# Kernel tuning notes

Hardware: AMD Instinct MI355X
Metric: run time of the kernel (lower is better)

## Reference

```python
import jax, jax.numpy as jnp
import numpy as np
import math

D_MODEL = 1024
N_HEADS = 16
D_HEAD = 64
VOCAB = 32000
MAX_SEQ = 2048
PAD_TOKEN = 0
EPS = 1e-5
NEG = -1000000000.0


def layer_norm(x, g, b):
    m = jnp.mean(x, axis=-1, keepdims=True)
    v = jnp.mean(jnp.square(x - m), axis=-1, keepdims=True)
    return (x - m) * jax.lax.rsqrt(v + EPS) * g + b


def setup_inputs() -> dict:
    key = jax.random.key(0)
    ks = jax.random.split(key, 12)
    s = 0.02
    inp = {
        "tokens": jax.random.randint(ks[0], (2, 2048), 0, VOCAB, dtype=jnp.int64)
            if jax.config.jax_enable_x64 else jax.random.randint(ks[0], (2, 2048), 0, VOCAB, dtype=jnp.int32),
        "emb": jax.random.normal(ks[1], (VOCAB, D_MODEL), jnp.float32) * s,
        "pos_emb": jax.random.normal(ks[2], (MAX_SEQ, D_MODEL), jnp.float32) * s,
        "ln1_g": jnp.ones((D_MODEL,), jnp.float32), "ln1_b": jnp.zeros((D_MODEL,), jnp.float32),
        "ln2_g": jnp.ones((D_MODEL,), jnp.float32), "ln2_b": jnp.zeros((D_MODEL,), jnp.float32),
        "ln3_g": jnp.ones((D_MODEL,), jnp.float32), "ln3_b": jnp.zeros((D_MODEL,), jnp.float32),
        "Wq": jax.random.normal(ks[3], (D_MODEL, N_HEADS * D_HEAD), jnp.float32) * s,
        "bq": jnp.zeros((N_HEADS * D_HEAD,), jnp.float32),
        "Wk": jax.random.normal(ks[4], (D_MODEL, N_HEADS * D_HEAD), jnp.float32) * s,
        "bk": jnp.zeros((N_HEADS * D_HEAD,), jnp.float32),
        "Wv": jax.random.normal(ks[5], (D_MODEL, N_HEADS * D_HEAD), jnp.float32) * s,
        "bv": jnp.zeros((N_HEADS * D_HEAD,), jnp.float32),
        "Wo": jax.random.normal(ks[6], (N_HEADS * D_HEAD, D_MODEL), jnp.float32) * s,
        "bo": jnp.zeros((D_MODEL,), jnp.float32),
        "W1": jax.random.normal(ks[7], (D_MODEL, 4 * D_MODEL), jnp.float32) * s,
        "b1": jnp.zeros((4 * D_MODEL,), jnp.float32),
        "W2": jax.random.normal(ks[8], (4 * D_MODEL, D_MODEL), jnp.float32) * s,
        "b2": jnp.zeros((D_MODEL,), jnp.float32),
    }
    return inp


def reference(tokens, emb, pos_emb, ln1_g, ln1_b, ln2_g, ln2_b, ln3_g, ln3_b,
              Wq, bq, Wk, bk, Wv, bv, Wo, bo, W1, b1, W2, b2):
    b, s = tokens.shape
    # embedding + learned positional embedding
    x = emb[tokens] + pos_emb[jnp.arange(s)][None, :, :]  # [b,s,d]
    x = layer_norm(x, ln1_g, ln1_b)
    Q = (x @ Wq + bq).reshape(b, s, N_HEADS, D_HEAD).transpose(0, 2, 1, 3)  # [b,n,s,d]
    K = (x @ Wk + bk).reshape(b, s, N_HEADS, D_HEAD).transpose(0, 2, 1, 3)
    V = (x @ Wv + bv).reshape(b, s, N_HEADS, D_HEAD).transpose(0, 2, 1, 3)
    logits = jnp.einsum('bnsd,bntd->bnst', Q, K) / math.sqrt(D_HEAD)  # [b,n,s,s]
    causal = jnp.triu(jnp.full((s, s), NEG, jnp.float32), k=1)
    pad_mask = jnp.where(tokens == PAD_TOKEN, NEG, 0.0)  # keys masked: [b,s]
    logits = logits + causal[None, None, :, :] + pad_mask[:, None, None, :]
    probs = jax.nn.softmax(logits, axis=-1)
    attn = jnp.einsum('bnst,bntd->bnsd', probs, V)
    attn = attn.transpose(0, 2, 1, 3).reshape(b, s, N_HEADS * D_HEAD)
    attn_out = attn @ Wo + bo
    x = x + layer_norm(attn_out, ln2_g, ln2_b)
    h = jax.nn.gelu(layer_norm(x, ln3_g, ln3_b) @ W1 + b1, approximate=False)
    x = x + (h @ W2 + b2)
    return x
```

## Files before the change

### kernel.cpp

```cpp
#include <hip/hip_runtime.h>
#include <cstdint>
#include <cstddef>


#define SEQ     2048
#define NTOK    4096
#define DMODEL  1024
#define NHEAD   16
#define DHEAD   64
#define MASKV   (-30.0f)
#define LN_EPS  1e-5f

typedef __bf16 bf16_t;
typedef __bf16 bf16x8 __attribute__((ext_vector_type(8)));
typedef float  f32x4  __attribute__((ext_vector_type(4)));

#define MFMA_BF16(a,b,c) __builtin_amdgcn_mfma_f32_16x16x32_bf16((a),(b),(c),0,0,0)

__device__ __forceinline__ void gload_lds16(const void* g, void* l) {
  __builtin_amdgcn_global_load_lds(
      (__attribute__((address_space(1))) void*)(g),
      (__attribute__((address_space(3))) void*)(l), 16, 0, 0);
}

__global__ __launch_bounds__(256)
void wtrans_kernel(const float* __restrict__ W, bf16_t* __restrict__ WT,
                   int K, int N) {
  __shared__ float tile[64][65];
  const int n0 = blockIdx.x * 64, k0 = blockIdx.y * 64;
  const int c = threadIdx.x & 63, rb = threadIdx.x >> 6;
#pragma unroll
  for (int i = 0; i < 16; ++i) {
    int r = i * 4 + rb;
    tile[r][c] = W[(size_t)(k0 + r) * N + n0 + c];
  }
  __syncthreads();
#pragma unroll
  for (int i = 0; i < 16; ++i) {
    int r = i * 4 + rb;
    WT[(size_t)(n0 + r) * K + k0 + c] = (bf16_t)tile[c][r];
  }
}

__global__ __launch_bounds__(256)
void pack_bias_kernel(const float* __restrict__ bq, const float* __restrict__ bk,
                      const float* __restrict__ bv, float* __restrict__ o) {
  int i = blockIdx.x * 256 + threadIdx.x;
  if (i < 1024) { o[i] = bq[i]; o[1024 + i] = bk[i]; o[2048 + i] = bv[i]; }
}

__global__ __launch_bounds__(256)
void ln1_kernel(const int* __restrict__ tokens, const float* __restrict__ emb,
                const float* __restrict__ pos, const float* __restrict__ g,
                const float* __restrict__ bb, float* __restrict__ xln,
                bf16_t* __restrict__ xlnb) {
  __shared__ float red[8];
  const int t = blockIdx.x;
  const int s = t & (SEQ - 1);
  const int tok = tokens[t];
  const int d0 = threadIdx.x * 4;
  const int w = threadIdx.x >> 6, lane = threadIdx.x & 63;

  float4 e  = *(const float4*)(emb + (size_t)tok * DMODEL + d0);
  float4 pp = *(const float4*)(pos + (size_t)s   * DMODEL + d0);
  float x0 = e.x + pp.x, x1 = e.y + pp.y, x2v = e.z + pp.z, x3v = e.w + pp.w;
  float s1 = x0 + x1 + x2v + x3v;
  float s2 = x0*x0 + x1*x1 + x2v*x2v + x3v*x3v;
#pragma unroll
  for (int o = 32; o >= 1; o >>= 1) { s1 += __shfl_xor(s1, o); s2 += __shfl_xor(s2, o); }
  if (lane == 0) { red[w] = s1; red[4 + w] = s2; }
  __syncthreads();
  s1 = red[0] + red[1] + red[2] + red[3];
  s2 = red[4] + red[5] + red[6] + red[7];
  float mean = s1 * (1.0f / DMODEL);
  float var  = s2 * (1.0f / DMODEL) - mean * mean;
  float inv  = rsqrtf(var + LN_EPS);
  float4 gv = *(const float4*)(g + d0);
  float4 bv = *(const float4*)(bb + d0);
  float y0 = (x0  - mean) * inv * gv.x + bv.x;
  float y1 = (x1  - mean) * inv * gv.y + bv.y;
  float y2 = (x2v - mean) * inv * gv.z + bv.z;
  float y3 = (x3v - mean) * inv * gv.w + bv.w;
  *(float4*)(xln + (size_t)t * DMODEL + d0) = make_float4(y0, y1, y2, y3);
  union { ushort4 u; bf16_t b[4]; } cv;
  cv.b[0] = (bf16_t)y0; cv.b[1] = (bf16_t)y1; cv.b[2] = (bf16_t)y2; cv.b[3] = (bf16_t)y3;
  *(ushort4*)(xlnb + (size_t)t * DMODEL + d0) = cv.u;
}

__global__ __launch_bounds__(256)
void ln23_kernel(const float* __restrict__ ao, const float* __restrict__ xln,
                 const float* __restrict__ g2, const float* __restrict__ bb2,
                 const float* __restrict__ g3, const float* __restrict__ bb3,
                 float* __restrict__ x2o, bf16_t* __restrict__ x3b) {
  __shared__ float red[8];
  const int t = blockIdx.x;
  const int d0 = threadIdx.x * 4;
  const int w = threadIdx.x >> 6, lane = threadIdx.x & 63;

  float4 a = *(const float4*)(ao + (size_t)t * DMODEL + d0);
  float s1 = a.x + a.y + a.z + a.w;
  float s2 = a.x*a.x + a.y*a.y + a.z*a.z + a.w*a.w;
#pragma unroll
  for (int o = 32; o >= 1; o >>= 1) { s1 += __shfl_xor(s1, o); s2 += __shfl_xor(s2, o); }
  if (lane == 0) { red[w] = s1; red[4 + w] = s2; }
  __syncthreads();
  s1 = red[0] + red[1] + red[2] + red[3];
  s2 = red[4] + red[5] + red[6] + red[7];
  float mean = s1 * (1.0f / DMODEL);
  float var  = s2 * (1.0f / DMODEL) - mean * mean;
  float inv  = rsqrtf(var + LN_EPS);
  float4 gv = *(const float4*)(g2 + d0);
  float4 bv = *(const float4*)(bb2 + d0);
  float4 xv = *(const float4*)(xln + (size_t)t * DMODEL + d0);
  float y0 = xv.x + (a.x - mean) * inv * gv.x + bv.x;
  float y1 = xv.y + (a.y - mean) * inv * gv.y + bv.y;
  float y2 = xv.z + (a.z - mean) * inv * gv.z + bv.z;
  float y3 = xv.w + (a.w - mean) * inv * gv.w + bv.w;
  *(float4*)(x2o + (size_t)t * DMODEL + d0) = make_float4(y0, y1, y2, y3);

  float t1 = y0 + y1 + y2 + y3;
  float t2 = y0*y0 + y1*y1 + y2*y2 + y3*y3;
#pragma unroll
  for (int o = 32; o >= 1; o >>= 1) { t1 += __shfl_xor(t1, o); t2 += __shfl_xor(t2, o); }
  __syncthreads();
  if (lane == 0) { red[w] = t1; red[4 + w] = t2; }
  __syncthreads();
  t1 = red[0] + red[1] + red[2] + red[3];
  t2 = red[4] + red[5] + red[6] + red[7];
  float mean2 = t1 * (1.0f / DMODEL);
  float var2  = t2 * (1.0f / DMODEL) - mean2 * mean2;
  float inv2  = rsqrtf(var2 + LN_EPS);
  float4 gv3 = *(const float4*)(g3 + d0);
  float4 bv3 = *(const float4*)(bb3 + d0);
  union { ushort4 u; bf16_t b[4]; } cv;
  cv.b[0] = (bf16_t)((y0 - mean2) * inv2 * gv3.x + bv3.x);
  cv.b[1] = (bf16_t)((y1 - mean2) * inv2 * gv3.y + bv3.y);
  cv.b[2] = (bf16_t)((y2 - mean2) * inv2 * gv3.z + bv3.z);
  cv.b[3] = (bf16_t)((y3 - mean2) * inv2 * gv3.w + bv3.w);
  *(ushort4*)(x3b + (size_t)t * DMODEL + d0) = cv.u;
}

constexpr int EPI_BF16 = 0, EPI_F32 = 1, EPI_GELU = 2, EPI_RES = 3;

template <int EPI>
__global__ __launch_bounds__(256, 2)
void gemm_bt(const bf16_t* __restrict__ A, const bf16_t* __restrict__ B,
             const float* __restrict__ bias, const float* __restrict__ res,
             bf16_t* __restrict__ obf, float* __restrict__ of32,
             int M, int N, int K) {
  __shared__ __attribute__((aligned(16))) bf16_t As[128 * 64];
  __shared__ __attribute__((aligned(16))) bf16_t Bs[128 * 64];
  const int tid = threadIdx.x;
  const int w = tid >> 6, lane = tid & 63;
  const int quad = lane >> 4, l16 = lane & 15;
  const int m0 = blockIdx.x * 128, n0 = blockIdx.y * 128;
  const int wm = (w >> 1) * 64, wn = (w & 1) * 64;
  const size_t Kz = (size_t)K;

  f32x4 acc[4][4] = {};

  const bf16_t* Ag = A + (size_t)(m0 + w * 32 + (lane >> 3)) * Kz + (lane & 7) * 8;
  const bf16_t* Bg = B + (size_t)(n0 + w * 32 + (lane >> 3)) * Kz + (lane & 7) * 8;
  bf16_t* Asw = &As[(w * 32) * 64];
  bf16_t* Bsw = &Bs[(w * 32) * 64];

  for (int k0 = 0; k0 < K; k0 += 64) {
#pragma unroll
    for (int i = 0; i < 4; ++i) {
      gload_lds16(Ag + (size_t)i * 8 * Kz + k0, Asw + i * 8 * 64);
      gload_lds16(Bg + (size_t)i * 8 * Kz + k0, Bsw + i * 8 * 64);
    }
    __syncthreads();
#pragma unroll
    for (int kc = 0; kc < 2; ++kc) {
      bf16x8 af[4], bfr[4];
#pragma unroll
      for (int i = 0; i < 4; ++i) {
        af[i]  = *(const bf16x8*)&As[(wm + i * 16 + l16) * 64 + kc * 32 + quad * 8];
        bfr[i] = *(const bf16x8*)&Bs[(wn + i * 16 + l16) * 64 + kc * 32 + quad * 8];
      }
#pragma unroll
      for (int mi = 0; mi < 4; ++mi)
#pragma unroll
        for (int ni = 0; ni < 4; ++ni)
          acc[mi][ni] = MFMA_BF16(af[mi], bfr[ni], acc[mi][ni]);
    }
    __syncthreads();
  }

#pragma unroll
  for (int ni = 0; ni < 4; ++ni) {
    const int col = n0 + wn + ni * 16 + l16;
    const float bv = bias[col];
#pragma unroll
    for (int mi = 0; mi < 4; ++mi) {
#pragma unroll
      for (int r = 0; r < 4; ++r) {
        const int row = m0 + wm + mi * 16 + quad * 4 + r;
        float v = acc[mi][ni][r] + bv;
        if constexpr (EPI == EPI_GELU)
          v = 0.5f * v * (1.0f + erff(v * 0.70710678118654752f));
        if constexpr (EPI == EPI_RES)
          v += res[(size_t)row * N + col];
        if constexpr (EPI == EPI_BF16 || EPI == EPI_GELU)
          obf[(size_t)row * N + col] = (bf16_t)v;
        else
          of32[(size_t)row * N + col] = v;
      }
    }
  }
}

__global__ __launch_bounds__(256)
void vtrans_kernel(const bf16_t* __restrict__ qkv, bf16_t* __restrict__ Vt) {
  __shared__ bf16_t tile[64][72];
  const int bh = blockIdx.y;
  const int b = bh >> 4, h = bh & 15;
  const int s0 = blockIdx.x * 64;
  const int c = threadIdx.x & 63, rb = threadIdx.x >> 6;
#pragma unroll
  for (int i = 0; i < 16; ++i) {
    int r = i * 4 + rb;
    tile[r][c] = qkv[(size_t)(b * SEQ + s0 + r) * 3072 + 2048 + h * 64 + c];
  }
  __syncthreads();
#pragma unroll
  for (int i = 0; i < 16; ++i) {
    int r = i * 4 + rb;
    Vt[((size_t)bh * 64 + r) * SEQ + s0 + c] = tile[c][r];
  }
}


__device__ __forceinline__ unsigned pack2_bf16(float e, float o) {
  union { bf16_t b; unsigned short s; } lo, hi;
  lo.b = (bf16_t)e; hi.b = (bf16_t)o;
  return (unsigned)lo.s | ((unsigned)hi.s << 16);
}

template <bool DIAG>
__device__ __forceinline__ void attn_tile(
    int k0, int chunkCnt, int w, int quad, int l16, int krow,
    const bf16_t* __restrict__ Kbase, const bf16_t* __restrict__ Vbase,
    const int* __restrict__ tokb,
    const bf16x8 (&qf)[2][2], bf16x8 onev,
    f32x4 (&oacc)[2][4], f32x4 (&lacc)[2]) {

  f32x4 sc0[8], sc1[8];

#pragma unroll
  for (int c = 0; c < 4; ++c)
    if (!DIAG || c < chunkCnt) {
      int4 t0 = *(const int4*)(tokb + k0 + 32 * c + 8 * quad);
      int4 t1 = *(const int4*)(tokb + k0 + 32 * c + 8 * quad + 4);
      f32x4 pe, po;
      pe[0] = (t0.x == 0) ? MASKV : 0.0f;
      po[0] = (t0.y == 0) ? MASKV : 0.0f;
      pe[1] = (t0.z == 0) ? MASKV : 0.0f;
      po[1] = (t0.w == 0) ? MASKV : 0.0f;
      pe[2] = (t1.x == 0) ? MASKV : 0.0f;
      po[2] = (t1.y == 0) ? MASKV : 0.0f;
      pe[3] = (t1.z == 0) ? MASKV : 0.0f;
      po[3] = (t1.w == 0) ? MASKV : 0.0f;
      sc0[2 * c] = pe; sc0[2 * c + 1] = po;
      sc1[2 * c] = pe; sc1[2 * c + 1] = po;
    }

#pragma unroll
  for (int kc = 0; kc < 2; ++kc)
#pragma unroll
    for (int ni = 0; ni < 8; ++ni)
      if (!DIAG || ni < 2 * chunkCnt) {
        bf16x8 kf = *(const bf16x8*)(Kbase
            + (size_t)(k0 + 32 * (ni >> 1) + (ni & 1) + krow) * 3072
            + kc * 32 + quad * 8);
        sc0[ni] = MFMA_BF16(kf, qf[0][kc], sc0[ni]);
        sc1[ni] = MFMA_BF16(kf, qf[1][kc], sc1[ni]);
      }

#pragma unroll
  for (int mi = 0; mi < 2; ++mi) {
    f32x4* sc = mi ? sc1 : sc0;
    const int ql = w * 32 + mi * 16 + l16;
#pragma unroll
    for (int ni = 0; ni < 8; ++ni)
      if (!DIAG || ni < 2 * chunkCnt) {
#pragma unroll
        for (int r = 0; r < 4; ++r) {
          float v = sc[ni][r];
          if (DIAG) {
            int keyl = 32 * (ni >> 1) + (ni & 1) + 8 * quad + 2 * r;
            if (keyl > ql) v += MASKV;
          }
          sc[ni][r] = __expf(v);
        }
      }
  }

#pragma unroll
  for (int c = 0; c < 4; ++c)
    if (!DIAG || c < chunkCnt) {
      union { unsigned u[4]; bf16x8 v; } pb0, pb1;
#pragma unroll
      for (int m = 0; m < 4; ++m) {
        pb0.u[m] = pack2_bf16(sc0[2 * c][m], sc0[2 * c + 1][m]);
        pb1.u[m] = pack2_bf16(sc1[2 * c][m], sc1[2 * c + 1][m]);
      }
      lacc[0] = MFMA_BF16(onev, pb0.v, lacc[0]);
      lacc[1] = MFMA_BF16(onev, pb1.v, lacc[1]);
#pragma unroll
      for (int nd = 0; nd < 4; ++nd) {
        bf16x8 vf = *(const bf16x8*)(Vbase
            + (size_t)(nd * 16 + l16) * SEQ + k0 + c * 32 + quad * 8);
        oacc[0][nd] = MFMA_BF16(vf, pb0.v, oacc[0][nd]);
        oacc[1][nd] = MFMA_BF16(vf, pb1.v, oacc[1][nd]);
      }
    }
}

__global__ __launch_bounds__(256, 2)
void attn_kernel(const bf16_t* __restrict__ qkv, const bf16_t* __restrict__ Vt,
                 const int* __restrict__ tokens, bf16_t* __restrict__ attnb) {
  const int tid = threadIdx.x;
  const int w = tid >> 6, lane = tid & 63;
  const int quad = lane >> 4, l16 = lane & 15;
  const int bh = blockIdx.x;
  const int by = (int)blockIdx.y;
  const int strip = (by < 8) ? (15 - by) : (by - 8);
  const int b = bh >> 4, h = bh & 15;
  const int ntiles = strip + 1;
  const int qrow0 = strip * 128 + w * 32;
  const int krow = ((l16 >> 2) << 3) + ((l16 & 3) << 1);

  const bf16_t* Kbase = qkv + (size_t)b * SEQ * 3072 + 1024 + h * 64;
  const bf16_t* Vbase = Vt + (size_t)bh * 64 * SEQ;
  const int*    tokb  = tokens + b * SEQ;

  bf16x8 qf[2][2];
#pragma unroll
  for (int mi = 0; mi < 2; ++mi) {
    const size_t trow = (size_t)(b * SEQ + qrow0 + mi * 16 + l16) * 3072 + h * 64;
    qf[mi][0] = *(const bf16x8*)(qkv + trow + quad * 8);
    qf[mi][1] = *(const bf16x8*)(qkv + trow + 32 + quad * 8);
  }
#pragma unroll
  for (int mi = 0; mi < 2; ++mi)
#pragma unroll
    for (int kc = 0; kc < 2; ++kc)
#pragma unroll
      for (int j = 0; j < 8; ++j)
        qf[mi][kc][j] = (bf16_t)((float)qf[mi][kc][j] * 0.125f);

  bf16x8 onev;
#pragma unroll
  for (int j = 0; j < 8; ++j) onev[j] = (bf16_t)1.0f;

  f32x4 oacc[2][4] = {};
  f32x4 lacc[2] = {};

  for (int kt = 0; kt < ntiles - 1; ++kt)
    attn_tile<false>(kt * 128, 4, w, quad, l16, krow,
                     Kbase, Vbase, tokb, qf, onev, oacc, lacc);
  attn_tile<true>((ntiles - 1) * 128, w + 1, w, quad, l16, krow,
                  Kbase, Vbase, tokb, qf, onev, oacc, lacc);

#pragma unroll
  for (int mi = 0; mi < 2; ++mi) {
    const float invl = 1.0f / lacc[mi][0];
    const size_t row =
        (size_t)(b * SEQ + qrow0 + mi * 16 + l16) * DMODEL + h * 64;
#pragma unroll
    for (int nd = 0; nd < 4; ++nd) {
      union { ushort4 u; bf16_t bv[4]; } cv;
#pragma unroll
      for (int r = 0; r < 4; ++r)
        cv.bv[r] = (bf16_t)(oacc[mi][nd][r] * invl);
      *(ushort4*)(attnb + row + nd * 16 + quad * 4) = cv.u;
    }
  }
}

extern "C" void kernel_launch(void* const* d_in, const int* in_sizes, int n_in,
                              void* d_out, int out_size, void* d_ws, size_t ws_size,
                              hipStream_t stream) {
  const int*   tokens = (const int*)d_in[0];
  const float* emb    = (const float*)d_in[1];
  const float* pos    = (const float*)d_in[2];
  const float* ln1g   = (const float*)d_in[3];
  const float* ln1b   = (const float*)d_in[4];
  const float* ln2g   = (const float*)d_in[5];
  const float* ln2b   = (const float*)d_in[6];
  const float* ln3g   = (const float*)d_in[7];
  const float* ln3b   = (const float*)d_in[8];
  const float* Wq     = (const float*)d_in[9];
  const float* bq     = (const float*)d_in[10];
  const float* Wk     = (const float*)d_in[11];
  const float* bk     = (const float*)d_in[12];
  const float* Wv     = (const float*)d_in[13];
  const float* bv     = (const float*)d_in[14];
  const float* Wo     = (const float*)d_in[15];
  const float* bo     = (const float*)d_in[16];
  const float* W1     = (const float*)d_in[17];
  const float* b1     = (const float*)d_in[18];
  const float* W2     = (const float*)d_in[19];
  const float* b2     = (const float*)d_in[20];
  float* out = (float*)d_out;

  char* p = (char*)d_ws;
  auto alloc = [&](size_t bytes) {
    char* q = p; p += (bytes + 255) & ~(size_t)255; return q;
  };
  float*  x_ln   = (float*)alloc((size_t)NTOK * DMODEL * 4);
  bf16_t* x_lnb  = (bf16_t*)alloc((size_t)NTOK * DMODEL * 2);
  bf16_t* WqkvT  = (bf16_t*)alloc((size_t)3072 * 1024 * 2);
  float*  bqkv   = (float*)alloc(3072 * 4);
  bf16_t* WoT    = (bf16_t*)alloc((size_t)1024 * 1024 * 2);
  bf16_t* W1T    = (bf16_t*)alloc((size_t)4096 * 1024 * 2);
  bf16_t* W2T    = (bf16_t*)alloc((size_t)1024 * 4096 * 2);
  bf16_t* qkvb   = (bf16_t*)alloc((size_t)NTOK * 3072 * 2);
  bf16_t* Vtb    = (bf16_t*)alloc((size_t)32 * 64 * SEQ * 2);
  bf16_t* attnb  = (bf16_t*)alloc((size_t)NTOK * DMODEL * 2);
  float*  attn_o = (float*)alloc((size_t)NTOK * DMODEL * 4);
  float*  x2     = (float*)alloc((size_t)NTOK * DMODEL * 4);
  bf16_t* x3b    = (bf16_t*)alloc((size_t)NTOK * DMODEL * 2);
  bf16_t* hbuf   = (bf16_t*)alloc((size_t)NTOK * 4096 * 2);

  wtrans_kernel<<<dim3(16, 16), 256, 0, stream>>>(Wq, WqkvT,                 1024, 1024);
  wtrans_kernel<<<dim3(16, 16), 256, 0, stream>>>(Wk, WqkvT + 1024ull * 1024, 1024, 1024);
  wtrans_kernel<<<dim3(16, 16), 256, 0, stream>>>(Wv, WqkvT + 2048ull * 1024, 1024, 1024);
  wtrans_kernel<<<dim3(16, 16), 256, 0, stream>>>(Wo, WoT, 1024, 1024);
  wtrans_kernel<<<dim3(64, 16), 256, 0, stream>>>(W1, W1T, 1024, 4096);
  wtrans_kernel<<<dim3(16, 64), 256, 0, stream>>>(W2, W2T, 4096, 1024);
  pack_bias_kernel<<<4, 256, 0, stream>>>(bq, bk, bv, bqkv);

  ln1_kernel<<<NTOK, 256, 0, stream>>>(tokens, emb, pos, ln1g, ln1b, x_ln, x_lnb);

  gemm_bt<EPI_BF16><<<dim3(32, 24), 256, 0, stream>>>(
      x_lnb, WqkvT, bqkv, nullptr, qkvb, nullptr, NTOK, 3072, 1024);

  vtrans_kernel<<<dim3(32, 32), 256, 0, stream>>>(qkvb, Vtb);

  attn_kernel<<<dim3(32, 16), 256, 0, stream>>>(qkvb, Vtb, tokens, attnb);

  gemm_bt<EPI_F32><<<dim3(32, 8), 256, 0, stream>>>(
      attnb, WoT, bo, nullptr, nullptr, attn_o, NTOK, 1024, 1024);

  ln23_kernel<<<NTOK, 256, 0, stream>>>(attn_o, x_ln, ln2g, ln2b, ln3g, ln3b, x2, x3b);

  gemm_bt<EPI_GELU><<<dim3(32, 32), 256, 0, stream>>>(
      x3b, W1T, b1, nullptr, hbuf, nullptr, NTOK, 4096, 1024);

  gemm_bt<EPI_RES><<<dim3(32, 8), 256, 0, stream>>>(
      hbuf, W2T, b2, x2, nullptr, out, NTOK, 1024, 4096);

  (void)in_sizes; (void)n_in; (void)out_size; (void)ws_size;
}
```

Before: 582.9 us.

## Stage K/V tiles in swizzled double-buffered LDS for attention

The attention kernel now copies each 128-key K tile and V^T tile into double-buffered LDS with asynchronous global-to-LDS loads. The next tile is prefetched while the current one is computed, and the per-wave redundant global reads are replaced by XOR-swizzled LDS reads. The V transpose kernel writes 128-key blocks in the matching swizzled layout with 16-byte stores. The pad mask is applied after QK instead of being used to seed the accumulators. In exchange, the kernel uses 64KB of LDS and adds a block barrier per tile, which may limit occupancy to 2 blocks per CU.

```diff
diff --git a/kernel.cpp b/kernel.cpp
--- a/kernel.cpp
+++ b/kernel.cpp
@@ -213,21 +213,26 @@
 
 __global__ __launch_bounds__(256)
 void vtrans_kernel(const bf16_t* __restrict__ qkv, bf16_t* __restrict__ Vt) {
-  __shared__ bf16_t tile[64][72];
+  __shared__ bf16_t tile[128][72];
   const int bh = blockIdx.y;
   const int b = bh >> 4, h = bh & 15;
-  const int s0 = blockIdx.x * 64;
+  const int s0 = blockIdx.x * 128;
   const int c = threadIdx.x & 63, rb = threadIdx.x >> 6;
 #pragma unroll
-  for (int i = 0; i < 16; ++i) {
+  for (int i = 0; i < 32; ++i) {
     int r = i * 4 + rb;
     tile[r][c] = qkv[(size_t)(b * SEQ + s0 + r) * 3072 + 2048 + h * 64 + c];
   }
   __syncthreads();
-#pragma unroll
-  for (int i = 0; i < 16; ++i) {
-    int r = i * 4 + rb;
-    Vt[((size_t)bh * 64 + r) * SEQ + s0 + c] = tile[c][r];
+  const int d = threadIdx.x >> 2;
+  const int k4 = threadIdx.x & 3;
+#pragma unroll
+  for (int kk = 0; kk < 4; ++kk) {
+    const int k = kk * 4 + k4;
+    union { uint4 u; bf16_t bv[8]; } vv;
+#pragma unroll
+    for (int e = 0; e < 8; ++e) vv.bv[e] = tile[k * 8 + e][d];
+    *(uint4*)(Vt + (size_t)(bh * 64 + d) * SEQ + s0 + ((k ^ (d & 7)) << 3)) = vv.u;
   }
 }
 
@@ -238,42 +243,39 @@
   return (unsigned)lo.s | ((unsigned)hi.s << 16);
 }
 
+__device__ __forceinline__ int tok_at(const int4& a, const int4& b, int j) {
+  switch (j) {
+    case 0: return a.x; case 1: return a.y; case 2: return a.z; case 3: return a.w;
+    case 4: return b.x; case 5: return b.y; case 6: return b.z; default: return b.w;
+  }
+}
+
 template <bool DIAG>
 __device__ __forceinline__ void attn_tile(
-    int k0, int chunkCnt, int w, int quad, int l16, int krow,
-    const bf16_t* __restrict__ Kbase, const bf16_t* __restrict__ Vbase,
+    const bf16_t* __restrict__ Ksb, const bf16_t* __restrict__ Vsb,
+    int k0, int chunkCnt, int w, int quad, int l16, int krow, int xr0,
     const int* __restrict__ tokb,
     const bf16x8 (&qf)[2][2], bf16x8 onev,
     f32x4 (&oacc)[2][4], f32x4 (&lacc)[2]) {
 
-  f32x4 sc0[8], sc1[8];
-
+  int4 tA[4], tB[4];
 #pragma unroll
   for (int c = 0; c < 4; ++c)
     if (!DIAG || c < chunkCnt) {
-      int4 t0 = *(const int4*)(tokb + k0 + 32 * c + 8 * quad);
-      int4 t1 = *(const int4*)(tokb + k0 + 32 * c + 8 * quad + 4);
-      f32x4 pe, po;
-      pe[0] = (t0.x == 0) ? MASKV : 0.0f;
-      po[0] = (t0.y == 0) ? MASKV : 0.0f;
-      pe[1] = (t0.z == 0) ? MASKV : 0.0f;
-      po[1] = (t0.w == 0) ? MASKV : 0.0f;
-      pe[2] = (t1.x == 0) ? MASKV : 0.0f;
-      po[2] = (t1.y == 0) ? MASKV : 0.0f;
-      pe[3] = (t1.z == 0) ? MASKV : 0.0f;
-      po[3] = (t1.w == 0) ? MASKV : 0.0f;
-      sc0[2 * c] = pe; sc0[2 * c + 1] = po;
-      sc1[2 * c] = pe; sc1[2 * c + 1] = po;
-    }
+      tA[c] = *(const int4*)(tokb + k0 + 32 * c + 8 * quad);
+      tB[c] = *(const int4*)(tokb + k0 + 32 * c + 8 * quad + 4);
+    }
+
+  f32x4 sc0[8] = {}, sc1[8] = {};
 
 #pragma unroll
   for (int kc = 0; kc < 2; ++kc)
 #pragma unroll
     for (int ni = 0; ni < 8; ++ni)
       if (!DIAG || ni < 2 * chunkCnt) {
-        bf16x8 kf = *(const bf16x8*)(Kbase
-            + (size_t)(k0 + 32 * (ni >> 1) + (ni & 1) + krow) * 3072
-            + kc * 32 + quad * 8);
+        const int r = 32 * (ni >> 1) + (ni & 1) + krow;
+        bf16x8 kf = *(const bf16x8*)&Ksb[r * 64
+            + (((kc * 4 + quad) ^ (xr0 + (ni & 1))) << 3)];
         sc0[ni] = MFMA_BF16(kf, qf[0][kc], sc0[ni]);
         sc1[ni] = MFMA_BF16(kf, qf[1][kc], sc1[ni]);
       }
@@ -285,11 +287,13 @@
 #pragma unroll
     for (int ni = 0; ni < 8; ++ni)
       if (!DIAG || ni < 2 * chunkCnt) {
+        const int c = ni >> 1, e = ni & 1;
 #pragma unroll
         for (int r = 0; r < 4; ++r) {
           float v = sc[ni][r];
+          if (tok_at(tA[c], tB[c], 2 * r + e) == 0) v += MASKV;
           if (DIAG) {
-            int keyl = 32 * (ni >> 1) + (ni & 1) + 8 * quad + 2 * r;
+            int keyl = 32 * c + e + 8 * quad + 2 * r;
             if (keyl > ql) v += MASKV;
           }
           sc[ni][r] = __expf(v);
@@ -310,8 +314,8 @@
       lacc[1] = MFMA_BF16(onev, pb1.v, lacc[1]);
 #pragma unroll
       for (int nd = 0; nd < 4; ++nd) {
-        bf16x8 vf = *(const bf16x8*)(Vbase
-            + (size_t)(nd * 16 + l16) * SEQ + k0 + c * 32 + quad * 8);
+        bf16x8 vf = *(const bf16x8*)&Vsb[(nd * 16 + l16) * 128
+            + (((c * 4 + quad) ^ (l16 & 7)) << 3)];
         oacc[0][nd] = MFMA_BF16(vf, pb0.v, oacc[0][nd]);
         oacc[1][nd] = MFMA_BF16(vf, pb1.v, oacc[1][nd]);
       }
@@ -321,6 +325,9 @@
 __global__ __launch_bounds__(256, 2)
 void attn_kernel(const bf16_t* __restrict__ qkv, const bf16_t* __restrict__ Vt,
                  const int* __restrict__ tokens, bf16_t* __restrict__ attnb) {
+  __shared__ __attribute__((aligned(16))) bf16_t Ks[2][128 * 64];
+  __shared__ __attribute__((aligned(16))) bf16_t Vs[2][64 * 128];
+
   const int tid = threadIdx.x;
   const int w = tid >> 6, lane = tid & 63;
   const int quad = lane >> 4, l16 = lane & 15;
@@ -331,6 +338,8 @@
   const int ntiles = strip + 1;
   const int qrow0 = strip * 128 + w * 32;
   const int krow = ((l16 >> 2) << 3) + ((l16 & 3) << 1);
+  const int xr0 = (l16 & 3) << 1;
+  const int sw_chunk = (lane & 7) ^ ((lane >> 3) & 7);
 
   const bf16_t* Kbase = qkv + (size_t)b * SEQ * 3072 + 1024 + h * 64;
   const bf16_t* Vbase = Vt + (size_t)bh * 64 * SEQ;
@@ -358,11 +367,35 @@
   f32x4 oacc[2][4] = {};
   f32x4 lacc[2] = {};
 
-  for (int kt = 0; kt < ntiles - 1; ++kt)
-    attn_tile<false>(kt * 128, 4, w, quad, l16, krow,
-                     Kbase, Vbase, tokb, qf, onev, oacc, lacc);
-  attn_tile<true>((ntiles - 1) * 128, w + 1, w, quad, l16, krow,
-                  Kbase, Vbase, tokb, qf, onev, oacc, lacc);
+  auto stage = [&](int bf, int k0) {
+    const bf16_t* Kg = Kbase + (size_t)(k0 + w * 32 + (lane >> 3)) * 3072
+                       + sw_chunk * 8;
+    bf16_t* Kl = &Ks[bf][(w * 32) * 64];
+#pragma unroll
+    for (int i = 0; i < 4; ++i)
+      gload_lds16(Kg + (size_t)i * 8 * 3072, Kl + i * 8 * 64);
+    const bf16_t* Vg = Vbase + (size_t)(w * 16 + (lane >> 4)) * SEQ + k0
+                       + (lane & 15) * 8;
+    bf16_t* Vl = &Vs[bf][(w * 16) * 128];
+#pragma unroll
+    for (int i = 0; i < 4; ++i)
+      gload_lds16(Vg + (size_t)i * 4 * SEQ, Vl + i * 4 * 128);
+  };
+
+  stage(0, 0);
+  __syncthreads();
+  int cur = 0;
+  for (int kt = 0; kt < ntiles; ++kt) {
+    if (kt + 1 < ntiles) stage(cur ^ 1, (kt + 1) * 128);
+    if (kt == ntiles - 1)
+      attn_tile<true>(Ks[cur], Vs[cur], kt * 128, w + 1, w, quad, l16,
+                      krow, xr0, tokb, qf, onev, oacc, lacc);
+    else
+      attn_tile<false>(Ks[cur], Vs[cur], kt * 128, 4, w, quad, l16,
+                       krow, xr0, tokb, qf, onev, oacc, lacc);
+    __syncthreads();
+    cur ^= 1;
+  }
 
 #pragma unroll
   for (int mi = 0; mi < 2; ++mi) {
@@ -438,7 +471,7 @@
   gemm_bt<EPI_BF16><<<dim3(32, 24), 256, 0, stream>>>(
       x_lnb, WqkvT, bqkv, nullptr, qkvb, nullptr, NTOK, 3072, 1024);
 
-  vtrans_kernel<<<dim3(32, 32), 256, 0, stream>>>(qkvb, Vtb);
+  vtrans_kernel<<<dim3(16, 32), 256, 0, stream>>>(qkvb, Vtb);
 
   attn_kernel<<<dim3(32, 16), 256, 0, stream>>>(qkvb, Vtb, tokens, attnb);
 
```

Result: faster. 524.1 us (-10.1%).
